# Kernel tuning notes

Measured on AMD Instinct MI355X. Metric: run time of the kernel, lower is better.

Reference implementation:

```python
import jax, jax.numpy as jnp
import numpy as np

NUM_HEADS = 16
WINDOW = 256  # local_window_size: query i attends keys in [i-WINDOW+1, i]


def setup_inputs() -> dict:
    key = jax.random.key(0)
    ks = jax.random.split(key, 7)
    B, L, D = 2, 2048, 1024
    s = 0.02  # typical init scale for projection weights
    return {
        "hidden_states": jax.random.normal(ks[0], (B, L, D), jnp.float32),
        "Wq": jax.random.normal(ks[1], (D, D), jnp.float32) * s,
        "bq": jnp.zeros((D,), jnp.float32),
        "Wk": jax.random.normal(ks[2], (D, D), jnp.float32) * s,
        "bk": jnp.zeros((D,), jnp.float32),
        "Wv": jax.random.normal(ks[3], (D, D), jnp.float32) * s,
        "bv": jnp.zeros((D,), jnp.float32),
    }


def reference(hidden_states, Wq, bq, Wk, bk, Wv, bv):
    B, L, D = hidden_states.shape
    H = NUM_HEADS
    dh = D // H

    def split_heads(x):  # [B,L,D] -> [B,H,L,dh]
        return x.reshape(B, L, H, dh).transpose(0, 2, 1, 3)

    q = split_heads(hidden_states @ Wq + bq)
    k = split_heads(hidden_states @ Wk + bk)
    v = split_heads(hidden_states @ Wv + bv)

    scores = jnp.einsum("bhqd,bhkd->bhqk", q, k) / jnp.sqrt(jnp.float32(dh))

    # causal sliding-window band: key j visible to query i iff i-WINDOW < j <= i
    i = jnp.arange(L)[:, None]
    j = jnp.arange(L)[None, :]
    band = (j <= i) & (j > i - WINDOW)
    scores = jnp.where(band, scores, -jnp.inf)

    probs = jax.nn.softmax(scores, axis=-1)  # dropout p=0 (eval)
    out = jnp.einsum("bhqk,bhkd->bhqd", probs, v)
    return out.transpose(0, 2, 1, 3).reshape(B, L, D)
```

## Files before the change

### kernel.cpp

```cpp
#include <hip/hip_runtime.h>
#include <hip/hip_bf16.h>
#include <stdint.h>
#include <math.h>

typedef __bf16 bf16;
typedef bf16  bf16x4  __attribute__((ext_vector_type(4)));
typedef bf16  bf16x8  __attribute__((ext_vector_type(8)));
typedef float floatx4 __attribute__((ext_vector_type(4)));

#define MFMA_16x16x32_BF16(a, b, c) \
  __builtin_amdgcn_mfma_f32_16x16x32_bf16((a), (b), (c), 0, 0, 0)

__device__ __forceinline__ void load_lds16(const void* g, void* l) {
  __builtin_amdgcn_global_load_lds(
      (const __attribute__((address_space(1))) unsigned int*)g,
      (__attribute__((address_space(3))) unsigned int*)l, 16, 0, 0);
}

#define LSEQ 2048
#define DMODEL 1024
#define NH 16
#define DH 64

__global__ void pack_all(const float4* __restrict__ x, uint16_t* __restrict__ y,
                         const float* __restrict__ Wq, const float* __restrict__ Wk,
                         const float* __restrict__ Wv, uint16_t* __restrict__ Wt) {
  const int bi = blockIdx.x;
  if (bi < 4096) {
    int i = bi * 256 + threadIdx.x;
    float4 f = x[i];
    bf16x4 v;
    v[0] = (bf16)f.x; v[1] = (bf16)f.y; v[2] = (bf16)f.z; v[3] = (bf16)f.w;
    *(bf16x4*)&y[(size_t)i * 4] = v;
    return;
  }
  __shared__ float tile[32][33];
  const int p = bi - 4096;
  const int z = p >> 10;
  const int rem = p & 1023;
  const int k0 = (rem >> 5) * 32, n0 = (rem & 31) * 32;
  const float* W = (z == 0) ? Wq : (z == 1) ? Wk : Wv;
  const int tx = threadIdx.x & 31, ty = threadIdx.x >> 5;
#pragma unroll
  for (int i = 0; i < 4; ++i)
    tile[ty + i * 8][tx] = W[(size_t)(k0 + ty + i * 8) * DMODEL + n0 + tx];
  __syncthreads();
  uint16_t* out = Wt + (size_t)z * DMODEL * DMODEL;
#pragma unroll
  for (int i = 0; i < 4; ++i)
    *(bf16*)&out[(size_t)(n0 + ty + i * 8) * DMODEL + k0 + tx] =
        (bf16)tile[tx][ty + i * 8];
}

__global__ __launch_bounds__(256, 2) void qkv_gemm(
    const uint16_t* __restrict__ A, const uint16_t* __restrict__ Wt,
    const float* __restrict__ bq, const float* __restrict__ bk,
    const float* __restrict__ bv,
    uint16_t* __restrict__ outq, uint16_t* __restrict__ outk,
    uint16_t* __restrict__ outvt) {
  __shared__ __attribute__((aligned(16))) uint16_t lds[40960];

  const int xcd = blockIdx.x & 7;
  const int i = blockIdx.x >> 3;
  const int m0 = (xcd * 4 + (i & 3)) * 128;
  const int n0 = (i >> 2) * 192;

  const int t = threadIdx.x;
  const int lane = t & 63;
  const int w = t >> 6;
  const int wm = (w >> 1) * 64;
  const int wn = (w & 1) * 96;
  const int col = lane & 15;
  const int quad = lane >> 4;

  floatx4 acc[4][6] = {};

  auto stage = [&](int kt, int bi) {
    const int k0 = kt * 64;
    uint16_t* base = &lds[bi * 20480];
#pragma unroll
    for (int c = 0; c < 10; ++c) {
      int chunk = t + c * 256;
      if (chunk < 1024) {
        int row = chunk >> 3, sl = chunk & 7;
        const uint16_t* g =
            A + (size_t)(m0 + row) * DMODEL + k0 + ((sl ^ (row & 7)) * 8);
        load_lds16(g, &base[chunk * 8]);
      } else {
        int cb = chunk - 1024;
        int row = cb >> 3, sl = cb & 7;
        int gc = n0 + row;
        const uint16_t* g = Wt + ((size_t)(gc >> 10) << 20) +
                            (size_t)(gc & 1023) * DMODEL + k0 +
                            ((sl ^ (row & 7)) * 8);
        load_lds16(g, &base[8192 + cb * 8]);
      }
    }
  };

  stage(0, 0);
  for (int kt = 0; kt < 16; ++kt) {
    const uint16_t* buf = &lds[(kt & 1) * 20480];

    asm volatile("s_waitcnt vmcnt(0)" ::: "memory");
    __builtin_amdgcn_s_barrier();
    __builtin_amdgcn_sched_barrier(0);
    if (kt < 15) stage(kt + 1, (kt + 1) & 1);
    __builtin_amdgcn_sched_barrier(0);

    bf16x8 a0[4], b0[6], a1[4], b1[6];
#pragma unroll
    for (int mi = 0; mi < 4; ++mi) {
      int r = wm + mi * 16 + col;
      a0[mi] = *(const bf16x8*)&buf[r * 64 + ((quad ^ (r & 7)) * 8)];
    }
#pragma unroll
    for (int nj = 0; nj < 6; ++nj) {
      int r = wn + nj * 16 + col;
      b0[nj] = *(const bf16x8*)&buf[8192 + r * 64 + ((quad ^ (r & 7)) * 8)];
    }
#pragma unroll
    for (int mi = 0; mi < 4; ++mi) {
      int r = wm + mi * 16 + col;
      a1[mi] = *(const bf16x8*)&buf[r * 64 + (((4 + quad) ^ (r & 7)) * 8)];
    }
#pragma unroll
    for (int nj = 0; nj < 6; ++nj) {
      int r = wn + nj * 16 + col;
      b1[nj] = *(const bf16x8*)&buf[8192 + r * 64 + (((4 + quad) ^ (r & 7)) * 8)];
    }

    __builtin_amdgcn_s_setprio(1);
#pragma unroll
    for (int mi = 0; mi < 4; ++mi)
#pragma unroll
      for (int nj = 0; nj < 6; ++nj)
        acc[mi][nj] = MFMA_16x16x32_BF16(a0[mi], b0[nj], acc[mi][nj]);
    __builtin_amdgcn_s_setprio(0);
    __builtin_amdgcn_s_setprio(1);
#pragma unroll
    for (int mi = 0; mi < 4; ++mi)
#pragma unroll
      for (int nj = 0; nj < 6; ++nj)
        acc[mi][nj] = MFMA_16x16x32_BF16(a1[mi], b1[nj], acc[mi][nj]);
    __builtin_amdgcn_s_setprio(0);
  }
  __builtin_amdgcn_s_barrier();

  const int bI = m0 >> 11, l0 = m0 & 2047;

#pragma unroll
  for (int nj = 0; nj < 6; ++nj) {
    int gc = n0 + wn + nj * 16 + col;
    int zz = gc >> 10, rem = gc & 1023;
    if (zz != 2) {
      const float* biasp = (zz == 0) ? bq : bk;
      uint16_t* outp = (zz == 0) ? outq : outk;
      const float scale = (zz == 0) ? 0.125f : 1.0f;
      float bb = biasp[rem];
      int h = rem >> 6, d = rem & 63;
#pragma unroll
      for (int mi = 0; mi < 4; ++mi) {
#pragma unroll
        for (int r = 0; r < 4; ++r) {
          int l = l0 + wm + mi * 16 + quad * 4 + r;
          *(bf16*)&outp[(((size_t)bI * NH + h) * LSEQ + l) * DH + d] =
              (bf16)((acc[mi][nj][r] + bb) * scale);
        }
      }
    }
  }

  const int c2 = 2048 - n0;
  if (c2 < 192) {
    const int lo2 = c2 < 0 ? 0 : c2;
    __syncthreads();
#pragma unroll
    for (int nj = 0; nj < 6; ++nj) {
      int nloc = wn + nj * 16 + col;
      int gc = n0 + nloc;
      if (gc >= 2048) {
        float bb = bv[gc - 2048];
#pragma unroll
        for (int mi = 0; mi < 4; ++mi) {
          int mb = wm + mi * 16 + quad * 4;
          int pp = (mb & ~31) | (((mb >> 2) & 3) << 3) | (((mb >> 4) & 1) << 2);
#pragma unroll
          for (int r = 0; r < 4; ++r)
            *(bf16*)&lds[nloc * 136 + pp + r] = (bf16)(acc[mi][nj][r] + bb);
        }
      }
    }
    __syncthreads();
    const int cnt = (192 - lo2) * 16;
    for (int idx = t; idx < cnt; idx += 256) {
      int nloc = lo2 + (idx >> 4), ch = idx & 15;
      int rem = n0 + nloc - 2048;
      int h = rem >> 6, d = rem & 63;
      uint16_t* dst =
          &outvt[(((size_t)bI * NH + h) * DH + d) * LSEQ + l0 + ch * 8];
      *(bf16x8*)dst = *(const bf16x8*)&lds[nloc * 136 + ch * 8];
    }
  }
}

__global__ __launch_bounds__(256, 4) void attn(
    const uint16_t* __restrict__ Q, const uint16_t* __restrict__ K,
    const uint16_t* __restrict__ Vt, float* __restrict__ out) {
  __shared__ __attribute__((aligned(16))) uint16_t kbuf[2][4096];
  __shared__ __attribute__((aligned(16))) uint16_t vbuf[2][4096];

  const int t = threadIdx.x;
  const int lane = t & 63;
  const int w = t >> 6;
  const int xcd = blockIdx.x & 7;
  const int slot = blockIdx.x >> 3;
  const int bh = xcd * 4 + (slot >> 5);
  const int q0 = (slot & 31) * 64;
  const int q0w = q0 + w * 16;
  const int b = bh >> 4, h = bh & 15;
  const uint16_t* Qp = Q + (size_t)bh * LSEQ * DH;
  const uint16_t* Kp = K + (size_t)bh * LSEQ * DH;
  const uint16_t* Vp = Vt + (size_t)bh * DH * LSEQ;
  const int col = lane & 15, quad = lane >> 4;

  bf16x8 qf0 = *(const bf16x8*)&Qp[(size_t)(q0w + col) * DH + quad * 8];
  bf16x8 qf1 = *(const bf16x8*)&Qp[(size_t)(q0w + col) * DH + 32 + quad * 8];

  bf16x8 ones;
#pragma unroll
  for (int u = 0; u < 8; ++u) ones[u] = (bf16)1.0f;

  const int c_start = (q0 < 256) ? ((256 - q0) >> 6) : 0;

  floatx4 o[4] = {};
  floatx4 lac = {0.f, 0.f, 0.f, 0.f};

  auto stage = [&](int c, int bi) {
    const int kc = q0 - 256 + 64 * c;
    int ci = w * 64 + lane;
    {
      int row = ci >> 3, s = ci & 7;
      const uint16_t* g = Kp + (size_t)(kc + row) * DH + ((s ^ (row & 7)) * 8);
      load_lds16(g, &kbuf[bi][w * 512]);
      int row2 = row + 32;
      const uint16_t* g2 = Kp + (size_t)(kc + row2) * DH + ((s ^ (row2 & 7)) * 8);
      load_lds16(g2, &kbuf[bi][2048 + w * 512]);
    }
    {
      int d = ci >> 3, s = ci & 7;
      const uint16_t* g = Vp + (size_t)d * LSEQ + kc + ((s ^ (d & 7)) * 8);
      load_lds16(g, &vbuf[bi][w * 512]);
      int d2 = d + 32;
      const uint16_t* g2 = Vp + (size_t)d2 * LSEQ + kc + ((s ^ (d2 & 7)) * 8);
      load_lds16(g2, &vbuf[bi][2048 + w * 512]);
    }
  };

  stage(c_start, c_start & 1);

  for (int c = c_start; c <= 4; ++c) {
    __syncthreads();
    if (c < 4) stage(c + 1, (c + 1) & 1);

    const int kc = q0 - 256 + 64 * c;
    const int hi = q0w + 15, lo = q0w - 255;
    if (kc <= hi && kc + 64 > lo) {
      const uint16_t* kb_ = kbuf[c & 1];
      const uint16_t* vb_ = vbuf[c & 1];

      floatx4 sT[4] = {{0,0,0,0},{0,0,0,0},{0,0,0,0},{0,0,0,0}};
      __builtin_amdgcn_s_setprio(1);
#pragma unroll
      for (int sub = 0; sub < 4; ++sub) {
        int r_ = sub * 16 + col;
        bf16x8 ka  = *(const bf16x8*)&kb_[r_ * 64 + ((quad ^ (r_ & 7)) * 8)];
        bf16x8 kb2 = *(const bf16x8*)&kb_[r_ * 64 + (((4 + quad) ^ (r_ & 7)) * 8)];
        sT[sub] = MFMA_16x16x32_BF16(ka, qf0, sT[sub]);
        sT[sub] = MFMA_16x16x32_BF16(kb2, qf1, sT[sub]);
      }
      __builtin_amdgcn_s_setprio(0);

      const bool needm = (kc < q0w - 240) | (kc + 63 > q0w);
      const int q = q0w + col;
      bf16x8 pb[2];
#pragma unroll
      for (int sel = 0; sel < 2; ++sel) {
#pragma unroll
        for (int sp = 0; sp < 2; ++sp) {
#pragma unroll
          for (int r = 0; r < 4; ++r) {
            float v = sT[sel * 2 + sp][r];
            if (needm) {
              int key = kc + sel * 32 + sp * 16 + quad * 4 + r;
              v = ((key <= q) & (key > q - 256)) ? v : -INFINITY;
            }
            pb[sel][sp * 4 + r] = (bf16)__expf(v);
          }
        }
      }

      __builtin_amdgcn_s_setprio(1);
#pragma unroll
      for (int nj = 0; nj < 4; ++nj) {
        int d = nj * 16 + col;
        bf16x8 va0 = *(const bf16x8*)&vb_[d * 64 + ((quad ^ (d & 7)) * 8)];
        bf16x8 va1 = *(const bf16x8*)&vb_[d * 64 + (((4 + quad) ^ (d & 7)) * 8)];
        o[nj] = MFMA_16x16x32_BF16(va0, pb[0], o[nj]);
        o[nj] = MFMA_16x16x32_BF16(va1, pb[1], o[nj]);
      }
      lac = MFMA_16x16x32_BF16(ones, pb[0], lac);
      lac = MFMA_16x16x32_BF16(ones, pb[1], lac);
      __builtin_amdgcn_s_setprio(0);
    }
  }

  float rinv = 1.0f / lac[0];
#pragma unroll
  for (int nj = 0; nj < 4; ++nj) {
    float4 v4;
    v4.x = o[nj][0] * rinv; v4.y = o[nj][1] * rinv;
    v4.z = o[nj][2] * rinv; v4.w = o[nj][3] * rinv;
    *(float4*)&out[((size_t)b * LSEQ + q0w + col) * DMODEL + h * DH + nj * 16 + quad * 4] = v4;
  }
}

extern "C" void kernel_launch(void* const* d_in, const int* in_sizes, int n_in,
                              void* d_out, int out_size, void* d_ws, size_t ws_size,
                              hipStream_t stream) {
  const float* hidden = (const float*)d_in[0];
  const float* Wq = (const float*)d_in[1];
  const float* bq = (const float*)d_in[2];
  const float* Wk = (const float*)d_in[3];
  const float* bk = (const float*)d_in[4];
  const float* Wv = (const float*)d_in[5];
  const float* bv = (const float*)d_in[6];
  float* out = (float*)d_out;

  char* ws = (char*)d_ws;
  uint16_t* hb  = (uint16_t*)(ws);
  uint16_t* Wt  = (uint16_t*)(ws + ((size_t)8  << 20));
  uint16_t* qb  = (uint16_t*)(ws + ((size_t)14 << 20));
  uint16_t* kb  = (uint16_t*)(ws + ((size_t)22 << 20));
  uint16_t* vtb = (uint16_t*)(ws + ((size_t)30 << 20));

  pack_all<<<7168, 256, 0, stream>>>((const float4*)hidden, hb, Wq, Wk, Wv, Wt);
  qkv_gemm<<<512, 256, 0, stream>>>(hb, Wt, bq, bk, bv, qb, kb, vtb);
  attn<<<1024, 256, 0, stream>>>(qb, kb, vtb, out);
}
```

Baseline: 128.0 us.

## Fuse fp32-to-bf16 activation conversion into QKV GEMM A-tile loading

```diff
diff --git a/kernel.cpp b/kernel.cpp
--- a/kernel.cpp
+++ b/kernel.cpp
@@ -22,20 +22,10 @@
 #define NH 16
 #define DH 64
 
-__global__ void pack_all(const float4* __restrict__ x, uint16_t* __restrict__ y,
-                         const float* __restrict__ Wq, const float* __restrict__ Wk,
-                         const float* __restrict__ Wv, uint16_t* __restrict__ Wt) {
-  const int bi = blockIdx.x;
-  if (bi < 4096) {
-    int i = bi * 256 + threadIdx.x;
-    float4 f = x[i];
-    bf16x4 v;
-    v[0] = (bf16)f.x; v[1] = (bf16)f.y; v[2] = (bf16)f.z; v[3] = (bf16)f.w;
-    *(bf16x4*)&y[(size_t)i * 4] = v;
-    return;
-  }
+__global__ void pack_w(const float* __restrict__ Wq, const float* __restrict__ Wk,
+                       const float* __restrict__ Wv, uint16_t* __restrict__ Wt) {
   __shared__ float tile[32][33];
-  const int p = bi - 4096;
+  const int p = blockIdx.x;
   const int z = p >> 10;
   const int rem = p & 1023;
   const int k0 = (rem >> 5) * 32, n0 = (rem & 31) * 32;
@@ -53,7 +43,8 @@
 }
 
 __global__ __launch_bounds__(256, 2) void qkv_gemm(
-    const uint16_t* __restrict__ A, const uint16_t* __restrict__ Wt,
+    const float* __restrict__ A,
+    const uint16_t* __restrict__ Wt,
     const float* __restrict__ bq, const float* __restrict__ bk,
     const float* __restrict__ bv,
     uint16_t* __restrict__ outq, uint16_t* __restrict__ outk,
@@ -75,37 +66,63 @@
 
   floatx4 acc[4][6] = {};
 
-  auto stage = [&](int kt, int bi) {
+  auto stageB = [&](int kt, int bi) {
     const int k0 = kt * 64;
     uint16_t* base = &lds[bi * 20480];
 #pragma unroll
-    for (int c = 0; c < 10; ++c) {
+    for (int c = 0; c < 6; ++c) {
+      int cb = t + c * 256;
+      int row = cb >> 3, sl = cb & 7;
+      int gc = n0 + row;
+      const uint16_t* g = Wt + ((size_t)(gc >> 10) << 20) +
+                          (size_t)(gc & 1023) * DMODEL + k0 +
+                          ((sl ^ (row & 7)) * 8);
+      load_lds16(g, &base[8192 + cb * 8]);
+    }
+  };
+  auto issueA = [&](int kt, float4* areg) {
+    const int k0 = kt * 64;
+#pragma unroll
+    for (int c = 0; c < 4; ++c) {
       int chunk = t + c * 256;
-      if (chunk < 1024) {
-        int row = chunk >> 3, sl = chunk & 7;
-        const uint16_t* g =
-            A + (size_t)(m0 + row) * DMODEL + k0 + ((sl ^ (row & 7)) * 8);
-        load_lds16(g, &base[chunk * 8]);
-      } else {
-        int cb = chunk - 1024;
-        int row = cb >> 3, sl = cb & 7;
-        int gc = n0 + row;
-        const uint16_t* g = Wt + ((size_t)(gc >> 10) << 20) +
-                            (size_t)(gc & 1023) * DMODEL + k0 +
-                            ((sl ^ (row & 7)) * 8);
-        load_lds16(g, &base[8192 + cb * 8]);
-      }
+      int row = chunk >> 3, sl = chunk & 7;
+      const float* g = A + (size_t)(m0 + row) * DMODEL + k0 + ((sl ^ (row & 7)) * 8);
+      areg[c * 2]     = *(const float4*)g;
+      areg[c * 2 + 1] = *(const float4*)(g + 4);
     }
   };
-
-  stage(0, 0);
+  auto writeA = [&](int bi, const float4* areg) {
+    uint16_t* base = &lds[bi * 20480];
+#pragma unroll
+    for (int c = 0; c < 4; ++c) {
+      int chunk = t + c * 256;
+      bf16x8 v;
+      v[0] = (bf16)areg[c * 2].x;     v[1] = (bf16)areg[c * 2].y;
+      v[2] = (bf16)areg[c * 2].z;     v[3] = (bf16)areg[c * 2].w;
+      v[4] = (bf16)areg[c * 2 + 1].x; v[5] = (bf16)areg[c * 2 + 1].y;
+      v[6] = (bf16)areg[c * 2 + 1].z; v[7] = (bf16)areg[c * 2 + 1].w;
+      *(bf16x8*)&base[chunk * 8] = v;
+    }
+  };
+
+  {
+    float4 areg[8];
+    issueA(0, areg);
+    writeA(0, areg);
+    stageB(0, 0);
+  }
+
   for (int kt = 0; kt < 16; ++kt) {
     const uint16_t* buf = &lds[(kt & 1) * 20480];
-
-    asm volatile("s_waitcnt vmcnt(0)" ::: "memory");
-    __builtin_amdgcn_s_barrier();
+    const int nbi = (kt + 1) & 1;
+
+    __syncthreads();
     __builtin_amdgcn_sched_barrier(0);
-    if (kt < 15) stage(kt + 1, (kt + 1) & 1);
+    float4 areg[8];
+    if (kt < 15) {
+      issueA(kt + 1, areg);
+      stageB(kt + 1, nbi);
+    }
     __builtin_amdgcn_sched_barrier(0);
 
     bf16x8 a0[4], b0[6], a1[4], b1[6];
@@ -137,6 +154,9 @@
       for (int nj = 0; nj < 6; ++nj)
         acc[mi][nj] = MFMA_16x16x32_BF16(a0[mi], b0[nj], acc[mi][nj]);
     __builtin_amdgcn_s_setprio(0);
+
+    if (kt < 15) writeA(nbi, areg);
+
     __builtin_amdgcn_s_setprio(1);
 #pragma unroll
     for (int mi = 0; mi < 4; ++mi)
@@ -145,7 +165,7 @@
         acc[mi][nj] = MFMA_16x16x32_BF16(a1[mi], b1[nj], acc[mi][nj]);
     __builtin_amdgcn_s_setprio(0);
   }
-  __builtin_amdgcn_s_barrier();
+  __syncthreads();
 
   const int bI = m0 >> 11, l0 = m0 & 2047;
 
@@ -338,13 +358,12 @@
   float* out = (float*)d_out;
 
   char* ws = (char*)d_ws;
-  uint16_t* hb  = (uint16_t*)(ws);
-  uint16_t* Wt  = (uint16_t*)(ws + ((size_t)8  << 20));
-  uint16_t* qb  = (uint16_t*)(ws + ((size_t)14 << 20));
-  uint16_t* kb  = (uint16_t*)(ws + ((size_t)22 << 20));
-  uint16_t* vtb = (uint16_t*)(ws + ((size_t)30 << 20));
-
-  pack_all<<<7168, 256, 0, stream>>>((const float4*)hidden, hb, Wq, Wk, Wv, Wt);
-  qkv_gemm<<<512, 256, 0, stream>>>(hb, Wt, bq, bk, bv, qb, kb, vtb);
+  uint16_t* Wt  = (uint16_t*)(ws);
+  uint16_t* qb  = (uint16_t*)(ws + ((size_t)6  << 20));
+  uint16_t* kb  = (uint16_t*)(ws + ((size_t)14 << 20));
+  uint16_t* vtb = (uint16_t*)(ws + ((size_t)22 << 20));
+
+  pack_w<<<3072, 256, 0, stream>>>(Wq, Wk, Wv, Wt);
+  qkv_gemm<<<512, 256, 0, stream>>>(hidden, Wt, bq, bk, bv, qb, kb, vtb);
   attn<<<1024, 256, 0, stream>>>(qb, kb, vtb, out);
 }
```

After: 133.3 us. 1.04x slower.
